# Optimization experiments

Measured on AMD Instinct MI355X. Metric: run time of the kernel, lower is better.

Reference implementation:

```python
import jax, jax.numpy as jnp
from jax import lax
import numpy as np

N, C_IN, C_OUT, H, W, DS = 32, 16, 1, 128, 128, 5
NC = C_OUT * C_IN  # channels fed to DUBlock convs (= out_nc*nc_d[0])


def autocorr(x, ds):
    """x:(N,C,H,W) -> xtx_raw:(N,C,C,2ds-1,2ds-1).
    xtx_raw[n,i,j,u,v] = sum_{h,w} x[n,i,h,w] * xpad[n,j,u+h,v+w]  (zero pad ds-1),
    matching torch cal_xtx (sample-wise conv3d of x with itself)."""
    n, c, h, w = x.shape
    p = ds - 1
    xp = jnp.pad(x, ((0, 0), (0, 0), (p, p), (p, p)))
    rows = []
    for u in range(2 * ds - 1):
        cols = [jnp.einsum('nihw,njhw->nij', x,
                           lax.slice(xp, (0, 0, u, v), (n, c, u + h, v + w)))
                for v in range(2 * ds - 1)]
        rows.append(jnp.stack(cols, axis=-1))
    return jnp.stack(rows, axis=-2)  # (N,C,C,K,K), K=2ds-1


def crosscorr(x, y, ds):
    """x:(N,Ci,H,W), y:(N,Co,H,W) -> xty:(N,Co,Ci,ds,ds)  (torch cal_xty, pad=(ds-1)//2)."""
    n, c, h, w = x.shape
    p = (ds - 1) // 2
    xp = jnp.pad(x, ((0, 0), (0, 0), (p, p), (p, p)))
    rows = []
    for u in range(ds):
        cols = [jnp.einsum('nohw,njhw->noj', y,
                           lax.slice(xp, (0, 0, u, v), (n, c, u + h, v + w)))
                for v in range(ds)]
        rows.append(jnp.stack(cols, axis=-1))
    return jnp.stack(rows, axis=-2)  # (N,Co,Ci,ds,ds)


def assemble_Q(R, ds):
    """Block-Toeplitz assembly. Equivalent to torch's unfold + flip + index permutation:
    Q[n,(i,p,q),(j,oi,oj)] = R[n,i,j, ds-1+oi-p, ds-1+oj-q]."""
    n, c = R.shape[0], R.shape[1]
    r = jnp.arange(ds)
    idx = (ds - 1) + r[None, :] - r[:, None]  # idx[p,o] = ds-1+o-p in [0, 2ds-2]
    Q6 = R[:, :, :, idx[:, None, :, None], idx[None, :, None, :]]  # (N,i,j,p,q,oi,oj)
    return jnp.transpose(Q6, (0, 1, 3, 4, 2, 5, 6)).reshape(n, c * ds * ds, c * ds * ds)


def dsb(x, d, y, alpha, reg):
    """DSBlock: regularized normal equations + batched SPD solve.
    x:(N,Ci,H,W), d:(N,Co,Ci,ds,ds), y:(N,Co,H,W), alpha:(N,1,1,1), reg:(1,)"""
    n, ci, h, w = x.shape
    co, ds = d.shape[1], d.shape[-1]
    Q = assemble_Q(autocorr(x, ds), ds)                               # (N, ci*ds^2, ci*ds^2)
    P = crosscorr(x, y, ds).reshape(n, co, -1).transpose(0, 2, 1)      # (N, ci*ds^2, co)
    a = alpha.reshape(n, 1, 1) * (h * w) * reg / (ds * ds * ci)        # (N,1,1)
    m = Q.shape[1]
    Q = Q + a * jnp.eye(m, dtype=Q.dtype)
    P = P + a * d.reshape(n, co, -1).transpose(0, 2, 1)
    # torch uses cholesky + cholesky_solve on SPD Q; jnp.linalg.solve computes the
    # same solution (and its vjp matches the custom CholeskySolve backward for symmetric Q).
    D = jnp.linalg.solve(Q, P)                                         # (N, ci*ds^2, co)
    return D.reshape(n, ci, ds, ds, co).transpose(0, 4, 1, 2, 3)       # (N,Co,Ci,ds,ds)


def conv3x3(x, wgt, b):
    o = lax.conv_general_dilated(x, wgt, (1, 1), ((1, 1), (1, 1)),
                                 dimension_numbers=('NCHW', 'OIHW', 'NCHW'))
    return o + b[None, :, None, None]


def dblock_fwd(x1, x2, d, y1, y2, alpha, beta, reg,
               w1, b1, w2, b2, w3, b3, w4, b4, w5, b5, w6, b6):
    d = dsb(x1, d, y1, alpha, reg)
    d = dsb(x2, d, y2, alpha, reg)
    n, co, ci, ds = d.shape[0], d.shape[1], d.shape[2], d.shape[3]
    bmap = jnp.broadcast_to(1.0 / jnp.sqrt(beta), (n, 1, ds, ds))      # (1/beta.sqrt()).repeat
    h0 = jnp.concatenate([d.reshape(n, co * ci, ds, ds), bmap], axis=1)
    # DUBlock
    t = jax.nn.relu(conv3x3(jax.nn.relu(conv3x3(h0, w1, b1)), w2, b2))
    t = jax.nn.relu(conv3x3(jax.nn.relu(conv3x3(t, w3, b3)), w4, b4))
    t = conv3x3(jax.nn.relu(conv3x3(t, w5, b5)), w6, b6) + h0[:, :-1]
    return t.reshape(n, co, ci, ds, ds)


def setup_inputs() -> dict:
    key = jax.random.key(0)
    ks = jax.random.split(key, 24)
    inp = {
        'x1': jax.random.normal(ks[0], (N, C_IN, H, W), jnp.float32),
        'x2': jax.random.normal(ks[1], (N, C_IN, H, W), jnp.float32),
        'd': jax.random.normal(ks[2], (N, C_OUT, C_IN, DS, DS), jnp.float32),
        'y1': jax.random.normal(ks[3], (N, C_OUT, H, W), jnp.float32),
        'y2': jax.random.normal(ks[4], (N, C_OUT, H, W), jnp.float32),
        'alpha': jax.random.uniform(ks[5], (N, 1, 1, 1), jnp.float32),
        'beta': jax.random.uniform(ks[6], (N, 1, 1, 1), jnp.float32),
        'reg': jnp.ones((1,), jnp.float32),
    }
    cins = [NC + 1, NC, NC, NC, NC, NC]
    for i in range(6):
        inp['w%d' % (i + 1)] = 0.05 * jax.random.normal(ks[7 + i], (NC, cins[i], 3, 3), jnp.float32)
        inp['b%d' % (i + 1)] = jnp.zeros((NC,), jnp.float32)
    return inp


def reference(x1, x2, d, y1, y2, alpha, beta, reg,
              w1, b1, w2, b2, w3, b3, w4, b4, w5, b5, w6, b6):
    return dblock_fwd(x1, x2, d, y1, y2, alpha, beta, reg,
                      w1, b1, w2, b2, w3, b3, w4, b4, w5, b5, w6, b6)
```

## Files before the change

### kernel.cpp

```cpp
#include <hip/hip_runtime.h>
#include <hip/hip_bf16.h>

constexpr int NS   = 32;
constexpr int C    = 16;
constexpr int H    = 128;
constexpr int W    = 128;
constexpr int DS   = 5;
constexpr int M    = C * DS * DS;
constexpr int NLAG = 81;

typedef short short8 __attribute__((ext_vector_type(8)));
typedef float f32x4 __attribute__((ext_vector_type(4)));

constexpr int CH_U    = 152;
constexpr int SLOT_U  = 16 * CH_U;
constexpr int SLOT_B  = SLOT_U * 2;
constexpr int RING_B  = 16 * SLOT_B;
constexpr int CHK     = 19;
constexpr size_t XB_US_PER_IN = (size_t)NS * H * 16 * CH_U;

__device__ __forceinline__ unsigned int pk_bf16(float a, float b) {
    union { __hip_bfloat162 h; unsigned int u; } cv;
    cv.h = __float22bfloat162_rn(make_float2(a, b));
    return cv.u;
}

__device__ __forceinline__ void gl_lds16(const void* g, void* l) {
    __builtin_amdgcn_global_load_lds(
        (const __attribute__((address_space(1))) unsigned int*)g,
        (__attribute__((address_space(3))) unsigned int*)l, 16, 0, 0);
}

__global__ __launch_bounds__(256, 1)
void prep_kernel(const float* __restrict__ x1, const float* __restrict__ x2,
                 const float* __restrict__ y1, const float* __restrict__ y2,
                 unsigned short* __restrict__ xb,
                 float* __restrict__ P1, float* __restrict__ P2)
{
    const int b = blockIdx.x, tid = threadIdx.x;
    if (b < 1024) {
        const int n = b & 31, zi = (b >> 5) & 1, rg = b >> 6;
        const float* xn = (zi ? x2 : x1) + (size_t)n * C * H * W;
        uint4* dst = (uint4*)(xb + (size_t)zi * XB_US_PER_IN +
                              ((size_t)n * H) * SLOT_U);
        for (int f = tid; f < 8 * 16 * CHK; f += 256) {
            const int rc = f / CHK, g = f - rc * CHK;
            const int row = rg * 8 + (rc >> 4), ch = rc & 15;
            uint4 o = make_uint4(0u, 0u, 0u, 0u);
            if (g >= 1 && g <= 16) {
                const float4* s4 = (const float4*)(xn + ((size_t)ch * H + row) * W + (g - 1) * 8);
                float4 va = s4[0], vb = s4[1];
                o.x = pk_bf16(va.x, va.y); o.y = pk_bf16(va.z, va.w);
                o.z = pk_bf16(vb.x, vb.y); o.w = pk_bf16(vb.z, vb.w);
            }
            dst[((size_t)row * 16 + ch) * CHK + g] = o;
        }
        return;
    }
    const int b2 = b - 1024;
    const int n = b2 & 31, j = (b2 >> 5) & 15, zi = b2 >> 9;
    const float* x = zi ? x2 : x1;
    const float* y = zi ? y2 : y1;
    float* P       = zi ? P2 : P1;

    const float* yn = y + (size_t)n * H * W;
    const float* xc = x + ((size_t)n * C + j) * H * W;

    const int wg = tid & 31, slab = tid >> 5;
    const int r0 = slab * 16;

    float acc[25];
#pragma unroll
    for (int l = 0; l < 25; ++l) acc[l] = 0.f;

    float4 yw[5];
#pragma unroll
    for (int u = 0; u < 5; ++u) {
        const int t = r0 + 1 - u;
        yw[u] = (t >= 0) ? *(const float4*)(yn + (size_t)t * W + wg * 4)
                         : make_float4(0.f, 0.f, 0.f, 0.f);
    }

#pragma unroll 4
    for (int rr = 0; rr < 16; ++rr) {
        const int r = r0 + rr;
#pragma unroll
        for (int u = 4; u >= 1; --u) yw[u] = yw[u - 1];
        const int tnew = r + 2;
        yw[0] = (tnew < H) ? *(const float4*)(yn + (size_t)tnew * W + wg * 4)
                           : make_float4(0.f, 0.f, 0.f, 0.f);

        const float* xr = xc + (size_t)r * W + wg * 4;
        float w12[12];
        float4 t4 = (wg > 0) ? *(const float4*)(xr - 4) : make_float4(0, 0, 0, 0);
        w12[0] = t4.x; w12[1] = t4.y; w12[2] = t4.z; w12[3] = t4.w;
        t4 = *(const float4*)(xr);
        w12[4] = t4.x; w12[5] = t4.y; w12[6] = t4.z; w12[7] = t4.w;
        t4 = (wg < 31) ? *(const float4*)(xr + 4) : make_float4(0, 0, 0, 0);
        w12[8] = t4.x; w12[9] = t4.y; w12[10] = t4.z; w12[11] = t4.w;

#pragma unroll
        for (int u = 0; u < 5; ++u) {
#pragma unroll
            for (int v = 0; v < 5; ++v)
                acc[u * 5 + v] += yw[u].x * w12[2 + v] + yw[u].y * w12[3 + v] +
                                  yw[u].z * w12[4 + v] + yw[u].w * w12[5 + v];
        }
    }

    __shared__ float red[4][25];
    const int lane = tid & 63, wv = tid >> 6;
#pragma unroll
    for (int l = 0; l < 25; ++l) {
        float v = acc[l];
#pragma unroll
        for (int off = 32; off; off >>= 1) v += __shfl_down(v, off);
        if (lane == 0) red[wv][l] = v;
    }
    __syncthreads();
    if (tid < 25)
        P[((size_t)n * C + j) * 25 + tid] = red[0][tid] + red[1][tid] + red[2][tid] + red[3][tid];
}

template<int P0, int P1>
__device__ __forceinline__ void autocorr_body(const unsigned short* __restrict__ xn,
                                              float* __restrict__ Rn,
                                              char* sm, int tid)
{
    constexpr int U0 = P0 / 9;
    constexpr int U1 = (P1 - 1) / 9;
    constexpr int NB = U1 - U0 + 1;
    constexpr int NP = P1 - P0;
    constexpr int SLOT_Q = SLOT_B / 16;

    unsigned short* ring = (unsigned short*)sm;
    const int lane = tid & 63;
    const int wid  = tid >> 6;
    const int q    = lane >> 4;
    const int mi   = lane & 15;
    const int rh   = wid & 3;
    const int chh  = wid >> 2;

    f32x4 acc[NP];
#pragma unroll
    for (int l = 0; l < NP; ++l) acc[l] = (f32x4){0.f, 0.f, 0.f, 0.f};

    const char* gb = (const char*)xn;

    for (int f = tid; f < 4 * SLOT_Q; f += 512)
        ((uint4*)sm)[(12 + f / SLOT_Q) * SLOT_Q + (f % SLOT_Q)] = make_uint4(0, 0, 0, 0);
    for (int f = wid; f < 38; f += 8)
        gl_lds16(gb + (size_t)f * 1024 + lane * 16, sm + f * 1024);
    __syncthreads();

    for (int s = 0; s < H; s += 4) {
        if (s < H - 8) {
            const size_t gbase = (size_t)(s + 8) * SLOT_B;
            char* lbase = sm + ((s + 8) & 15) * SLOT_B;
            for (int f = wid; f < 19; f += 8)
                gl_lds16(gb + gbase + (size_t)f * 1024 + lane * 16, lbase + f * 1024);
        } else {
            for (int f = tid; f < 4 * SLOT_Q; f += 512)
                ((uint4*)sm)[(((s + 8 + f / SLOT_Q) & 15)) * SLOT_Q + (f % SLOT_Q)] = make_uint4(0, 0, 0, 0);
        }

        const int r = s + rh;
        const unsigned short* rowA = ring + (r & 15) * SLOT_U + mi * CH_U;
#pragma unroll
        for (int cc = 0; cc < 2; ++cc) {
            const int w0 = (chh * 2 + cc) * 32;
            const uint4* pa = (const uint4*)(rowA + w0 + 8 * q);
            uint4 A0 = pa[0], A1 = pa[1], A2 = pa[2];
            unsigned int d[12] = {A0.x, A0.y, A0.z, A0.w, A1.x, A1.y, A1.z, A1.w,
                                  A2.x, A2.y, A2.z, A2.w};
            short8 bf[NB];
#pragma unroll
            for (int u = U0; u <= U1; ++u)
                bf[u - U0] = *(const short8*)(ring + ((r + u - 4 + 16) & 15) * SLOT_U +
                                              mi * CH_U + 8 + w0 + 8 * q);
#pragma unroll
            for (int v = 0; v < 9; ++v) {
                const int off = 12 - v;
                const int q4  = off >> 1;
                union { unsigned int u4[4]; short8 s8; } af;
                if (off & 1) {
#pragma unroll
                    for (int k2 = 0; k2 < 4; ++k2)
                        af.u4[k2] = (d[q4 + k2] >> 16) | (d[q4 + k2 + 1] << 16);
                } else {
#pragma unroll
                    for (int k2 = 0; k2 < 4; ++k2) af.u4[k2] = d[q4 + k2];
                }
#pragma unroll
                for (int u = U0; u <= U1; ++u) {
                    if (u * 9 + v >= P0 && u * 9 + v < P1)
                        acc[u * 9 + v - P0] = __builtin_amdgcn_mfma_f32_16x16x32_bf16(
                            af.s8, bf[u - U0], acc[u * 9 + v - P0], 0, 0, 0);
                }
            }
        }
        __syncthreads();
    }

    float* sred = (float*)sm;
#pragma unroll
    for (int cb = 0; cb < NP; cb += 9) {
        const int nc = (NP - cb < 9) ? (NP - cb) : 9;
        __syncthreads();
#pragma unroll
        for (int pp = 0; pp < 9; ++pp) {
            if (pp < nc) {
#pragma unroll
                for (int rg = 0; rg < 4; ++rg)
                    sred[(pp * 8 + wid) * 256 + (q * 4 + rg) * 16 + mi] = acc[cb + pp][rg];
            }
        }
        __syncthreads();
        if (tid < 256) {
#pragma unroll
            for (int pp = 0; pp < 9; ++pp) {
                if (pp < nc) {
                    float ssum = 0.f;
#pragma unroll
                    for (int w8 = 0; w8 < 8; ++w8)
                        ssum += sred[(pp * 8 + w8) * 256 + tid];
                    Rn[(size_t)tid * NLAG + P0 + cb + pp] = ssum;
                }
            }
        }
    }
}

__global__ __launch_bounds__(512, 2)
void autocorr_mfma(const unsigned short* __restrict__ xb,
                   float* __restrict__ R1, float* __restrict__ R2)
{
    __shared__ __align__(16) char sm[RING_B];
    const int n = blockIdx.x, zi = blockIdx.y, ug = blockIdx.z;
    const unsigned short* xn = xb + (size_t)zi * XB_US_PER_IN + (size_t)n * H * SLOT_U;
    float* Rn = (zi ? R2 : R1) + (size_t)n * C * C * NLAG;
    switch (ug) {
        case 0:  autocorr_body< 0, 20>(xn, Rn, sm, threadIdx.x); break;
        case 1:  autocorr_body<20, 40>(xn, Rn, sm, threadIdx.x); break;
        case 2:  autocorr_body<40, 60>(xn, Rn, sm, threadIdx.x); break;
        default: autocorr_body<60, 81>(xn, Rn, sm, threadIdx.x); break;
    }
}

__device__ __forceinline__ float block_sum512(float v, float* red, int tid)
{
#pragma unroll
    for (int off = 32; off; off >>= 1) v += __shfl_down(v, off);
    if ((tid & 63) == 0) red[tid >> 6] = v;
    __syncthreads();
    float s = red[0] + red[1] + red[2] + red[3] + red[4] + red[5] + red[6] + red[7];
    __syncthreads();
    return s;
}

__device__ __forceinline__ float cg_solve(const float* __restrict__ Rrow, float rhs,
                                          int iters, float a, int t,
                                          float* pv, float* ap, float* red)
{
    const int jj = t & 15;
    float zreg = 0.f, rreg = 0.f, pmine = 0.f;
    if (t < M) {
        rreg = rhs; pmine = rhs;
        pv[(t / 25) * 28 + (t % 25)] = rhs;
    }
    float rr = block_sum512((t < M) ? rreg * rreg : 0.f, red, t);

    for (int it = 0; it < iters; ++it) {
        if (t < 256) {
            float pld[25], acc[25];
            const float* pj = &pv[jj * 28];
#pragma unroll
            for (int k = 0; k < 25; ++k) pld[k] = pj[k];
#pragma unroll
            for (int k = 0; k < 25; ++k) acc[k] = 0.f;
#pragma unroll
            for (int u = 0; u < 9; ++u) {
#pragma unroll
                for (int v = 0; v < 9; ++v) {
                    const float Rv = Rrow[u * 9 + v];
#pragma unroll
                    for (int c = 0; c < 5; ++c) {
                        if (c < u - 4 || c > u) continue;
                        const int aa = 4 + c - u;
#pragma unroll
                        for (int dd = 0; dd < 5; ++dd) {
                            if (dd < v - 4 || dd > v) continue;
                            const int bb = 4 + dd - v;
                            acc[aa * 5 + bb] += Rv * pld[c * 5 + dd];
                        }
                    }
                }
            }
#pragma unroll
            for (int k = 0; k < 25; ++k) {
                float s2 = acc[k];
                s2 += __shfl_down(s2, 8, 16);
                s2 += __shfl_down(s2, 4, 16);
                s2 += __shfl_down(s2, 2, 16);
                s2 += __shfl_down(s2, 1, 16);
                acc[k] = s2;
            }
            if (jj == 0) {
#pragma unroll
                for (int k = 0; k < 25; ++k) ap[(t >> 4) * 25 + k] = acc[k];
            }
        }
        __syncthreads();
        float apv = 0.f;
        if (t < M) apv = ap[t] + a * pmine;
        float pAp = block_sum512((t < M) ? pmine * apv : 0.f, red, t);
        float al  = (pAp > 1e-30f) ? rr / pAp : 0.f;
        if (t < M) { zreg += al * pmine; rreg -= al * apv; }
        float rrn = block_sum512(rreg * rreg, red, t);
        float be  = (rr > 1e-30f) ? rrn / rr : 0.f;
        rr = rrn;
        if (t < M) {
            pmine = rreg + be * pmine;
            pv[(t / 25) * 28 + (t % 25)] = pmine;
        }
        __syncthreads();
    }
    return zreg;
}

__global__ __launch_bounds__(512, 1)
void solve_kernel(const float* __restrict__ R1, const float* __restrict__ R2,
                  const float* __restrict__ P1, const float* __restrict__ P2,
                  const float* __restrict__ d0, const float* __restrict__ alpha,
                  const float* __restrict__ beta, const float* __restrict__ reg,
                  const float* __restrict__ w1, const float* __restrict__ b1,
                  const float* __restrict__ w2, const float* __restrict__ b2,
                  const float* __restrict__ w3, const float* __restrict__ b3,
                  const float* __restrict__ w4, const float* __restrict__ b4,
                  const float* __restrict__ w5, const float* __restrict__ b5,
                  const float* __restrict__ w6, const float* __restrict__ b6,
                  float* __restrict__ out)
{
    __shared__ __align__(16) float Rl[256 * NLAG];
    __shared__ float pv[16 * 28];
    __shared__ float ap[M];
    __shared__ float red[8];
    __shared__ float h0p[25 * 20];
    __shared__ float bufA[25 * 20], bufB[25 * 20];
    __shared__ float wl[16 * 9 * 20];
    __shared__ float bl[16];

    const int n = blockIdx.x, t = threadIdx.x;
    const float a = alpha[n] * (float)(H * W) * reg[0] / (float)(DS * DS * C);

    {
        const char* g = (const char*)(R1 + (size_t)n * 256 * NLAG);
        char* l = (char*)Rl;
        for (int f = t; f < 256 * NLAG / 4; f += 512)
            gl_lds16(g + (size_t)f * 16, l + (size_t)f * 16);
    }
    float rhs1 = 0.f;
    if (t < M) rhs1 = P1[(size_t)n * M + t] + a * d0[(size_t)n * M + t];
    __syncthreads();
    float z1 = cg_solve(&Rl[(t & 255) * NLAG], rhs1, 3, a, t, pv, ap, red);

    __syncthreads();
    {
        const char* g = (const char*)(R2 + (size_t)n * 256 * NLAG);
        char* l = (char*)Rl;
        for (int f = t; f < 256 * NLAG / 4; f += 512)
            gl_lds16(g + (size_t)f * 16, l + (size_t)f * 16);
    }
    float rhs2 = 0.f;
    if (t < M) rhs2 = P2[(size_t)n * M + t] + a * z1;
    __syncthreads();
    float z2 = cg_solve(&Rl[(t & 255) * NLAG], rhs2, 7, a, t, pv, ap, red);

    if (t < M) h0p[(t % 25) * 20 + t / 25] = z2;
    if (t < 25) h0p[t * 20 + 16] = rsqrtf(beta[n]);
    __syncthreads();

    const float* wsl[6] = {w1, w2, w3, w4, w5, w6};
    const float* bsl[6] = {b1, b2, b3, b4, b5, b6};

    for (int l = 0; l < 6; ++l) {
        const int cin = (l == 0) ? 17 : 16;
        for (int f = t; f < 16 * cin * 9; f += 512) {
            const int o = f / (cin * 9);
            const int rm = f - o * cin * 9;
            const int ci = rm / 9, kk = rm - ci * 9;
            wl[(o * 9 + kk) * 20 + ci] = wsl[l][f];
        }
        if (t < 16) bl[t] = bsl[l][t];
        __syncthreads();

        const float* act = (l == 0) ? h0p : ((l & 1) ? bufA : bufB);
        float s = 0.f;
        if (t < 400) {
            const int o = t / 25, pix = t % 25, yy = pix / 5, xx = pix % 5;
            s = bl[o];
#pragma unroll
            for (int ky = 0; ky < 3; ++ky) {
                const int iy = yy + ky - 1;
                if ((unsigned)iy >= 5u) continue;
#pragma unroll
                for (int kx = 0; kx < 3; ++kx) {
                    const int ix = xx + kx - 1;
                    if ((unsigned)ix >= 5u) continue;
                    const float* ip = act + (iy * 5 + ix) * 20;
                    const float* wp = wl + (o * 9 + ky * 3 + kx) * 20;
                    const float4 a0 = *(const float4*)(ip);
                    const float4 a1 = *(const float4*)(ip + 4);
                    const float4 a2 = *(const float4*)(ip + 8);
                    const float4 a3 = *(const float4*)(ip + 12);
                    const float4 q0 = *(const float4*)(wp);
                    const float4 q1 = *(const float4*)(wp + 4);
                    const float4 q2 = *(const float4*)(wp + 8);
                    const float4 q3 = *(const float4*)(wp + 12);
                    s += a0.x * q0.x + a0.y * q0.y + a0.z * q0.z + a0.w * q0.w
                       + a1.x * q1.x + a1.y * q1.y + a1.z * q1.z + a1.w * q1.w
                       + a2.x * q2.x + a2.y * q2.y + a2.z * q2.z + a2.w * q2.w
                       + a3.x * q3.x + a3.y * q3.y + a3.z * q3.z + a3.w * q3.w;
                    if (l == 0) s += ip[16] * wp[16];
                }
            }
            if (l < 5) s = fmaxf(s, 0.f);
            else       s += h0p[(t % 25) * 20 + t / 25];
        }
        __syncthreads();
        if (t < 400) {
            if (l == 5) out[(size_t)n * M + t] = s;
            else {
                float* dstb = (l & 1) ? bufB : bufA;
                dstb[(t % 25) * 20 + t / 25] = s;
            }
        }
        __syncthreads();
    }
}

extern "C" void kernel_launch(void* const* d_in, const int* in_sizes, int n_in,
                              void* d_out, int out_size, void* d_ws, size_t ws_size,
                              hipStream_t stream)
{
    (void)in_sizes; (void)n_in; (void)out_size; (void)ws_size;
    const float* x1    = (const float*)d_in[0];
    const float* x2    = (const float*)d_in[1];
    const float* d0    = (const float*)d_in[2];
    const float* y1    = (const float*)d_in[3];
    const float* y2    = (const float*)d_in[4];
    const float* alpha = (const float*)d_in[5];
    const float* beta  = (const float*)d_in[6];
    const float* reg   = (const float*)d_in[7];
    const float* w1 = (const float*)d_in[8];  const float* b1 = (const float*)d_in[9];
    const float* w2 = (const float*)d_in[10]; const float* b2 = (const float*)d_in[11];
    const float* w3 = (const float*)d_in[12]; const float* b3 = (const float*)d_in[13];
    const float* w4 = (const float*)d_in[14]; const float* b4 = (const float*)d_in[15];
    const float* w5 = (const float*)d_in[16]; const float* b5 = (const float*)d_in[17];
    const float* w6 = (const float*)d_in[18]; const float* b6 = (const float*)d_in[19];
    float* out = (float*)d_out;

    char* wsb = (char*)d_ws;
    unsigned short* xb = (unsigned short*)wsb;
    float* R1 = (float*)(wsb + 2 * XB_US_PER_IN * 2);
    const size_t RSZ = (size_t)NS * C * C * NLAG;
    float* R2 = R1 + RSZ;
    float* P1 = R2 + RSZ;
    float* P2 = P1 + (size_t)NS * M;

    prep_kernel<<<2048, 256, 0, stream>>>(x1, x2, y1, y2, xb, P1, P2);
    autocorr_mfma<<<dim3(NS, 2, 4), 512, 0, stream>>>(xb, R1, R2);
    solve_kernel<<<NS, 512, 0, stream>>>(R1, R2, P1, P2, d0, alpha, beta, reg,
                                         w1, b1, w2, b2, w3, b3, w4, b4,
                                         w5, b5, w6, b6, out);
}
```

Measured before the change: 265.8 us.

## Cache R rows in registers, prefetch next operands during CG, fuse CG reductions

Each thread now copies its 81 R lags into registers, so the R2 load into LDS and later the pre-transformed conv weights can be issued asynchronously while the CG solve runs. The CG loop merges its two block reductions into one by computing pAp and w·w together and deriving the new residual norm algebraically. Conv weight reordering moves to an extra prep_kernel block that writes a global buffer, which removes the per-layer weight-transpose barriers from the solve kernel. The costs are much higher register pressure, since 81 floats are held per thread, and a residual recurrence that is less numerically stable.

```diff
diff --git a/kernel.cpp b/kernel.cpp
--- a/kernel.cpp
+++ b/kernel.cpp
@@ -19,6 +19,9 @@
 constexpr int CHK     = 19;
 constexpr size_t XB_US_PER_IN = (size_t)NS * H * 16 * CH_U;
 
+constexpr int WREP_F  = 6 * 144 * 20 + 6 * 16;
+constexpr int WREP_CH = WREP_F * 4 / 16;
+
 __device__ __forceinline__ unsigned int pk_bf16(float a, float b) {
     union { __hip_bfloat162 h; unsigned int u; } cv;
     cv.h = __float22bfloat162_rn(make_float2(a, b));
@@ -35,7 +38,14 @@
 void prep_kernel(const float* __restrict__ x1, const float* __restrict__ x2,
                  const float* __restrict__ y1, const float* __restrict__ y2,
                  unsigned short* __restrict__ xb,
-                 float* __restrict__ P1, float* __restrict__ P2)
+                 float* __restrict__ P1, float* __restrict__ P2,
+                 const float* __restrict__ w1, const float* __restrict__ b1,
+                 const float* __restrict__ w2, const float* __restrict__ b2,
+                 const float* __restrict__ w3, const float* __restrict__ b3,
+                 const float* __restrict__ w4, const float* __restrict__ b4,
+                 const float* __restrict__ w5, const float* __restrict__ b5,
+                 const float* __restrict__ w6, const float* __restrict__ b6,
+                 float* __restrict__ wrep)
 {
     const int b = blockIdx.x, tid = threadIdx.x;
     if (b < 1024) {
@@ -57,69 +67,86 @@
         }
         return;
     }
-    const int b2 = b - 1024;
-    const int n = b2 & 31, j = (b2 >> 5) & 15, zi = b2 >> 9;
-    const float* x = zi ? x2 : x1;
-    const float* y = zi ? y2 : y1;
-    float* P       = zi ? P2 : P1;
-
-    const float* yn = y + (size_t)n * H * W;
-    const float* xc = x + ((size_t)n * C + j) * H * W;
-
-    const int wg = tid & 31, slab = tid >> 5;
-    const int r0 = slab * 16;
-
-    float acc[25];
-#pragma unroll
-    for (int l = 0; l < 25; ++l) acc[l] = 0.f;
-
-    float4 yw[5];
-#pragma unroll
-    for (int u = 0; u < 5; ++u) {
-        const int t = r0 + 1 - u;
-        yw[u] = (t >= 0) ? *(const float4*)(yn + (size_t)t * W + wg * 4)
-                         : make_float4(0.f, 0.f, 0.f, 0.f);
-    }
+    if (b < 2048) {
+        const int b2 = b - 1024;
+        const int n = b2 & 31, j = (b2 >> 5) & 15, zi = b2 >> 9;
+        const float* x = zi ? x2 : x1;
+        const float* y = zi ? y2 : y1;
+        float* P       = zi ? P2 : P1;
+
+        const float* yn = y + (size_t)n * H * W;
+        const float* xc = x + ((size_t)n * C + j) * H * W;
+
+        const int wg = tid & 31, slab = tid >> 5;
+        const int r0 = slab * 16;
+
+        float acc[25];
+#pragma unroll
+        for (int l = 0; l < 25; ++l) acc[l] = 0.f;
+
+        float4 yw[5];
+#pragma unroll
+        for (int u = 0; u < 5; ++u) {
+            const int t = r0 + 1 - u;
+            yw[u] = (t >= 0) ? *(const float4*)(yn + (size_t)t * W + wg * 4)
+                             : make_float4(0.f, 0.f, 0.f, 0.f);
+        }
 
 #pragma unroll 4
-    for (int rr = 0; rr < 16; ++rr) {
-        const int r = r0 + rr;
-#pragma unroll
-        for (int u = 4; u >= 1; --u) yw[u] = yw[u - 1];
-        const int tnew = r + 2;
-        yw[0] = (tnew < H) ? *(const float4*)(yn + (size_t)tnew * W + wg * 4)
-                           : make_float4(0.f, 0.f, 0.f, 0.f);
-
-        const float* xr = xc + (size_t)r * W + wg * 4;
-        float w12[12];
-        float4 t4 = (wg > 0) ? *(const float4*)(xr - 4) : make_float4(0, 0, 0, 0);
-        w12[0] = t4.x; w12[1] = t4.y; w12[2] = t4.z; w12[3] = t4.w;
-        t4 = *(const float4*)(xr);
-        w12[4] = t4.x; w12[5] = t4.y; w12[6] = t4.z; w12[7] = t4.w;
-        t4 = (wg < 31) ? *(const float4*)(xr + 4) : make_float4(0, 0, 0, 0);
-        w12[8] = t4.x; w12[9] = t4.y; w12[10] = t4.z; w12[11] = t4.w;
-
-#pragma unroll
-        for (int u = 0; u < 5; ++u) {
-#pragma unroll
-            for (int v = 0; v < 5; ++v)
-                acc[u * 5 + v] += yw[u].x * w12[2 + v] + yw[u].y * w12[3 + v] +
-                                  yw[u].z * w12[4 + v] + yw[u].w * w12[5 + v];
-        }
-    }
-
-    __shared__ float red[4][25];
-    const int lane = tid & 63, wv = tid >> 6;
-#pragma unroll
-    for (int l = 0; l < 25; ++l) {
-        float v = acc[l];
-#pragma unroll
-        for (int off = 32; off; off >>= 1) v += __shfl_down(v, off);
-        if (lane == 0) red[wv][l] = v;
-    }
-    __syncthreads();
-    if (tid < 25)
-        P[((size_t)n * C + j) * 25 + tid] = red[0][tid] + red[1][tid] + red[2][tid] + red[3][tid];
+        for (int rr = 0; rr < 16; ++rr) {
+            const int r = r0 + rr;
+#pragma unroll
+            for (int u = 4; u >= 1; --u) yw[u] = yw[u - 1];
+            const int tnew = r + 2;
+            yw[0] = (tnew < H) ? *(const float4*)(yn + (size_t)tnew * W + wg * 4)
+                               : make_float4(0.f, 0.f, 0.f, 0.f);
+
+            const float* xr = xc + (size_t)r * W + wg * 4;
+            float w12[12];
+            float4 t4 = (wg > 0) ? *(const float4*)(xr - 4) : make_float4(0, 0, 0, 0);
+            w12[0] = t4.x; w12[1] = t4.y; w12[2] = t4.z; w12[3] = t4.w;
+            t4 = *(const float4*)(xr);
+            w12[4] = t4.x; w12[5] = t4.y; w12[6] = t4.z; w12[7] = t4.w;
+            t4 = (wg < 31) ? *(const float4*)(xr + 4) : make_float4(0, 0, 0, 0);
+            w12[8] = t4.x; w12[9] = t4.y; w12[10] = t4.z; w12[11] = t4.w;
+
+#pragma unroll
+            for (int u = 0; u < 5; ++u) {
+#pragma unroll
+                for (int v = 0; v < 5; ++v)
+                    acc[u * 5 + v] += yw[u].x * w12[2 + v] + yw[u].y * w12[3 + v] +
+                                      yw[u].z * w12[4 + v] + yw[u].w * w12[5 + v];
+            }
+        }
+
+        __shared__ float red[4][25];
+        const int lane = tid & 63, wv = tid >> 6;
+#pragma unroll
+        for (int l = 0; l < 25; ++l) {
+            float v = acc[l];
+#pragma unroll
+            for (int off = 32; off; off >>= 1) v += __shfl_down(v, off);
+            if (lane == 0) red[wv][l] = v;
+        }
+        __syncthreads();
+        if (tid < 25)
+            P[((size_t)n * C + j) * 25 + tid] = red[0][tid] + red[1][tid] + red[2][tid] + red[3][tid];
+        return;
+    }
+    const float* wsl[6] = {w1, w2, w3, w4, w5, w6};
+    const float* bsl[6] = {b1, b2, b3, b4, b5, b6};
+#pragma unroll
+    for (int l = 0; l < 6; ++l) {
+        const int cin = (l == 0) ? 17 : 16;
+        const float* ws = wsl[l];
+        for (int f = tid; f < 16 * cin * 9; f += 256) {
+            const int o = f / (cin * 9);
+            const int rm = f - o * cin * 9;
+            const int ci = rm / 9, kk = rm - ci * 9;
+            wrep[l * 2880 + (o * 9 + kk) * 20 + ci] = ws[f];
+        }
+        if (tid < 16) wrep[17280 + l * 16 + tid] = bsl[l][tid];
+    }
 }
 
 template<int P0, int P1>
@@ -258,7 +285,20 @@
     return s;
 }
 
-__device__ __forceinline__ float cg_solve(const float* __restrict__ Rrow, float rhs,
+__device__ __forceinline__ float2 block_sum512_f2(float v0, float v1, float* red, int tid)
+{
+#pragma unroll
+    for (int off = 32; off; off >>= 1) { v0 += __shfl_down(v0, off); v1 += __shfl_down(v1, off); }
+    if ((tid & 63) == 0) { red[(tid >> 6) * 2] = v0; red[(tid >> 6) * 2 + 1] = v1; }
+    __syncthreads();
+    float s0 = 0.f, s1 = 0.f;
+#pragma unroll
+    for (int i = 0; i < 8; ++i) { s0 += red[2 * i]; s1 += red[2 * i + 1]; }
+    __syncthreads();
+    return make_float2(s0, s1);
+}
+
+__device__ __forceinline__ float cg_solve(const float (&Rreg)[81], float rhs,
                                           int iters, float a, int t,
                                           float* pv, float* ap, float* red)
 {
@@ -282,7 +322,7 @@
             for (int u = 0; u < 9; ++u) {
 #pragma unroll
                 for (int v = 0; v < 9; ++v) {
-                    const float Rv = Rrow[u * 9 + v];
+                    const float Rv = Rreg[u * 9 + v];
 #pragma unroll
                     for (int c = 0; c < 5; ++c) {
                         if (c < u - 4 || c > u) continue;
@@ -311,15 +351,19 @@
             }
         }
         __syncthreads();
-        float apv = 0.f;
-        if (t < M) apv = ap[t] + a * pmine;
-        float pAp = block_sum512((t < M) ? pmine * apv : 0.f, red, t);
-        float al  = (pAp > 1e-30f) ? rr / pAp : 0.f;
-        if (t < M) { zreg += al * pmine; rreg -= al * apv; }
-        float rrn = block_sum512(rreg * rreg, red, t);
-        float be  = (rr > 1e-30f) ? rrn / rr : 0.f;
+        float wv = 0.f;
+        if (t < M) wv = ap[t] + a * pmine;
+        const float2 dots = block_sum512_f2((t < M) ? pmine * wv : 0.f,
+                                            (t < M) ? wv * wv : 0.f, red, t);
+        const float pAp = dots.x, ww = dots.y;
+        const bool ok = (pAp > 1e-30f);
+        const float al  = ok ? rr / pAp : 0.f;
+        float rrn = ok ? fmaxf(al * al * ww - rr, 0.f) : rr;
+        const float be  = (rr > 1e-30f) ? rrn / rr : 0.f;
         rr = rrn;
         if (t < M) {
+            zreg += al * pmine;
+            rreg -= al * wv;
             pmine = rreg + be * pmine;
             pv[(t / 25) * 28 + (t % 25)] = pmine;
         }
@@ -333,22 +377,15 @@
                   const float* __restrict__ P1, const float* __restrict__ P2,
                   const float* __restrict__ d0, const float* __restrict__ alpha,
                   const float* __restrict__ beta, const float* __restrict__ reg,
-                  const float* __restrict__ w1, const float* __restrict__ b1,
-                  const float* __restrict__ w2, const float* __restrict__ b2,
-                  const float* __restrict__ w3, const float* __restrict__ b3,
-                  const float* __restrict__ w4, const float* __restrict__ b4,
-                  const float* __restrict__ w5, const float* __restrict__ b5,
-                  const float* __restrict__ w6, const float* __restrict__ b6,
+                  const float* __restrict__ wrep,
                   float* __restrict__ out)
 {
     __shared__ __align__(16) float Rl[256 * NLAG];
     __shared__ float pv[16 * 28];
     __shared__ float ap[M];
-    __shared__ float red[8];
+    __shared__ float red[16];
     __shared__ float h0p[25 * 20];
     __shared__ float bufA[25 * 20], bufB[25 * 20];
-    __shared__ float wl[16 * 9 * 20];
-    __shared__ float bl[16];
 
     const int n = blockIdx.x, t = threadIdx.x;
     const float a = alpha[n] * (float)(H * W) * reg[0] / (float)(DS * DS * C);
@@ -356,49 +393,57 @@
     {
         const char* g = (const char*)(R1 + (size_t)n * 256 * NLAG);
         char* l = (char*)Rl;
-        for (int f = t; f < 256 * NLAG / 4; f += 512)
+        for (int f = t; f < 5184; f += 512)
             gl_lds16(g + (size_t)f * 16, l + (size_t)f * 16);
     }
     float rhs1 = 0.f;
     if (t < M) rhs1 = P1[(size_t)n * M + t] + a * d0[(size_t)n * M + t];
     __syncthreads();
-    float z1 = cg_solve(&Rl[(t & 255) * NLAG], rhs1, 3, a, t, pv, ap, red);
-
-    __syncthreads();
+
+    float Rreg[81];
+    {
+        const float* Rrow = &Rl[(t & 255) * NLAG];
+#pragma unroll
+        for (int i = 0; i < 81; ++i) Rreg[i] = Rrow[i];
+    }
+    __syncthreads();
+
     {
         const char* g = (const char*)(R2 + (size_t)n * 256 * NLAG);
         char* l = (char*)Rl;
-        for (int f = t; f < 256 * NLAG / 4; f += 512)
+        for (int f = t; f < 5184; f += 512)
+            gl_lds16(g + (size_t)f * 16, l + (size_t)f * 16);
+    }
+    float z1 = cg_solve(Rreg, rhs1, 3, a, t, pv, ap, red);
+    {
+        const float* Rrow = &Rl[(t & 255) * NLAG];
+#pragma unroll
+        for (int i = 0; i < 81; ++i) Rreg[i] = Rrow[i];
+    }
+    __syncthreads();
+
+    {
+        const char* g = (const char*)wrep;
+        char* l = (char*)Rl;
+        for (int f = t; f < WREP_CH; f += 512)
             gl_lds16(g + (size_t)f * 16, l + (size_t)f * 16);
     }
     float rhs2 = 0.f;
     if (t < M) rhs2 = P2[(size_t)n * M + t] + a * z1;
-    __syncthreads();
-    float z2 = cg_solve(&Rl[(t & 255) * NLAG], rhs2, 7, a, t, pv, ap, red);
-
+    float z2 = cg_solve(Rreg, rhs2, 7, a, t, pv, ap, red);
+
+    const float* wall = (const float*)Rl;
     if (t < M) h0p[(t % 25) * 20 + t / 25] = z2;
     if (t < 25) h0p[t * 20 + 16] = rsqrtf(beta[n]);
     __syncthreads();
 
-    const float* wsl[6] = {w1, w2, w3, w4, w5, w6};
-    const float* bsl[6] = {b1, b2, b3, b4, b5, b6};
-
+#pragma unroll
     for (int l = 0; l < 6; ++l) {
-        const int cin = (l == 0) ? 17 : 16;
-        for (int f = t; f < 16 * cin * 9; f += 512) {
-            const int o = f / (cin * 9);
-            const int rm = f - o * cin * 9;
-            const int ci = rm / 9, kk = rm - ci * 9;
-            wl[(o * 9 + kk) * 20 + ci] = wsl[l][f];
-        }
-        if (t < 16) bl[t] = bsl[l][t];
-        __syncthreads();
-
         const float* act = (l == 0) ? h0p : ((l & 1) ? bufA : bufB);
         float s = 0.f;
         if (t < 400) {
             const int o = t / 25, pix = t % 25, yy = pix / 5, xx = pix % 5;
-            s = bl[o];
+            s = wall[17280 + l * 16 + o];
 #pragma unroll
             for (int ky = 0; ky < 3; ++ky) {
                 const int iy = yy + ky - 1;
@@ -408,7 +453,7 @@
                     const int ix = xx + kx - 1;
                     if ((unsigned)ix >= 5u) continue;
                     const float* ip = act + (iy * 5 + ix) * 20;
-                    const float* wp = wl + (o * 9 + ky * 3 + kx) * 20;
+                    const float* wp = wall + l * 2880 + (o * 9 + ky * 3 + kx) * 20;
                     const float4 a0 = *(const float4*)(ip);
                     const float4 a1 = *(const float4*)(ip + 4);
                     const float4 a2 = *(const float4*)(ip + 8);
@@ -427,7 +472,6 @@
             if (l < 5) s = fmaxf(s, 0.f);
             else       s += h0p[(t % 25) * 20 + t / 25];
         }
-        __syncthreads();
         if (t < 400) {
             if (l == 5) out[(size_t)n * M + t] = s;
             else {
@@ -467,10 +511,12 @@
     float* R2 = R1 + RSZ;
     float* P1 = R2 + RSZ;
     float* P2 = P1 + (size_t)NS * M;
-
-    prep_kernel<<<2048, 256, 0, stream>>>(x1, x2, y1, y2, xb, P1, P2);
+    float* wrep = P2 + (size_t)NS * M;
+
+    prep_kernel<<<2049, 256, 0, stream>>>(x1, x2, y1, y2, xb, P1, P2,
+                                          w1, b1, w2, b2, w3, b3, w4, b4,
+                                          w5, b5, w6, b6, wrep);
     autocorr_mfma<<<dim3(NS, 2, 4), 512, 0, stream>>>(xb, R1, R2);
     solve_kernel<<<NS, 512, 0, stream>>>(R1, R2, P1, P2, d0, alpha, beta, reg,
-                                         w1, b1, w2, b2, w3, b3, w4, b4,
-                                         w5, b5, w6, b6, out);
-}
+                                         wrep, out);
+}
```

After: 291.1 us. +9.5%, slower.
